# Performance work log

Hardware: AMD Instinct MI355X
Metric: run time of the kernel (lower is better)

## Reference

```python
import jax, jax.numpy as jnp
import numpy as np

D_MODEL = 1024
NUM_HEADS = 16
D_K = D_MODEL // NUM_HEADS


def setup_inputs() -> dict:
    key = jax.random.key(0)
    k1, k2, k3, kq, kk, kv, ko = jax.random.split(key, 7)
    B, S = 4, 2048
    scale = 1.0 / np.sqrt(D_MODEL)
    return {
        "Q_in": jax.random.normal(k1, (B, S, D_MODEL), dtype=jnp.float32),
        "K_in": jax.random.normal(k2, (B, S, D_MODEL), dtype=jnp.float32),
        "V_in": jax.random.normal(k3, (B, S, D_MODEL), dtype=jnp.float32),
        "W_q": jax.random.normal(kq, (D_MODEL, D_MODEL), dtype=jnp.float32) * scale,
        "W_k": jax.random.normal(kk, (D_MODEL, D_MODEL), dtype=jnp.float32) * scale,
        "W_v": jax.random.normal(kv, (D_MODEL, D_MODEL), dtype=jnp.float32) * scale,
        "W_o": jax.random.normal(ko, (D_MODEL, D_MODEL), dtype=jnp.float32) * scale,
    }


def _split_heads(x):
    B, S, _ = x.shape
    return x.reshape(B, S, NUM_HEADS, D_K).transpose(0, 2, 1, 3)  # [B,H,S,d_k]


def reference(Q_in, K_in, V_in, W_q, W_k, W_v, W_o):
    # nn.Linear: y = x @ W.T ; here W_* stored as [out, in] equivalent square,
    # use x @ W.T convention to match torch.
    Q = _split_heads(Q_in @ W_q.T)
    K = _split_heads(K_in @ W_k.T)
    V = _split_heads(V_in @ W_v.T)
    scores = jnp.einsum("bhqd,bhkd->bhqk", Q, K) / jnp.sqrt(jnp.float32(D_K))
    attn = jax.nn.softmax(scores, axis=-1)  # [B,H,S,S]
    out = jnp.einsum("bhqk,bhkd->bhqd", attn, V)
    B, H, S, dk = out.shape
    concat = out.transpose(0, 2, 1, 3).reshape(B, S, H * dk)
    return concat @ W_o.T
```

## Files before the change

kernel.cpp:

```cpp
#include <hip/hip_runtime.h>
#include <math.h>

typedef __bf16 bf16x8v __attribute__((ext_vector_type(8)));
typedef float f32x4 __attribute__((ext_vector_type(4)));
typedef float f32x16 __attribute__((ext_vector_type(16)));

__device__ __forceinline__ void async_copy16(void* lds, const void* g) {
  __builtin_amdgcn_global_load_lds(
      (const __attribute__((address_space(1))) void*)g,
      (__attribute__((address_space(3))) void*)lds, 16, 0, 0);
}

struct CastArgs {
  const float* s[7];
  __bf16* d[7];
};
__global__ __launch_bounds__(256) void cast_kernel(CastArgs a) {
  const int t = blockIdx.y;
  const int n = (t < 3) ? 8388608 : 1048576;
  const int i = (blockIdx.x * 256 + threadIdx.x) * 8;
  if (i >= n) return;
  const float4 v0 = *(const float4*)(a.s[t] + i);
  const float4 v1 = *(const float4*)(a.s[t] + i + 4);
  bf16x8v o;
  o[0] = (__bf16)v0.x; o[1] = (__bf16)v0.y; o[2] = (__bf16)v0.z; o[3] = (__bf16)v0.w;
  o[4] = (__bf16)v1.x; o[5] = (__bf16)v1.y; o[6] = (__bf16)v1.z; o[7] = (__bf16)v1.w;
  *(bf16x8v*)(a.d[t] + i) = o;
}

template <int MODE, typename OutT>
__global__ __launch_bounds__(256) void gemm_bt(const __bf16* A, const __bf16* B,
                                               OutT* C,
                                               const __bf16* A2, const __bf16* B2,
                                               OutT* C2,
                                               int M, int N, int K) {
  __shared__ __bf16 As[128 * 64];
  __shared__ __bf16 Bs[128 * 64];
  if (blockIdx.z == 1) { A = A2; B = B2; C = C2; }
  const int tid = threadIdx.x;
  const int wave = tid >> 6, lane = tid & 63;
  const int lgrp = lane >> 4, lmod = lane & 15;
  const int bm = (MODE == 3 ? blockIdx.y : blockIdx.x) * 128;
  const int bn = (MODE == 3 ? blockIdx.x : blockIdx.y) * 128;
  const int wm = (wave >> 1) * 64, wn = (wave & 1) * 64;

  f32x4 acc[4][4];
#pragma unroll
  for (int mi = 0; mi < 4; mi++)
#pragma unroll
    for (int ni = 0; ni < 4; ni++)
#pragma unroll
      for (int r = 0; r < 4; r++) acc[mi][ni][r] = 0.f;

  for (int kt = 0; kt < K; kt += 64) {
#pragma unroll
    for (int i = 0; i < 4; i++) {
      const int s = i * 256 + tid;
      const int r = s >> 3, cb = s & 7;
      const int gc = (cb ^ (r & 7)) * 8;
      async_copy16(&As[s * 8], &A[(size_t)(bm + r) * K + kt + gc]);
      async_copy16(&Bs[s * 8], &B[(size_t)(bn + r) * K + kt + gc]);
    }
    __syncthreads();
#pragma unroll
    for (int ks = 0; ks < 2; ks++) {
      bf16x8v af[4], bf[4];
#pragma unroll
      for (int mi = 0; mi < 4; mi++) {
        const int row = wm + mi * 16 + lmod;
        af[mi] = *(const bf16x8v*)&As[row * 64 + ((ks * 4 + lgrp) ^ (row & 7)) * 8];
      }
#pragma unroll
      for (int ni = 0; ni < 4; ni++) {
        const int row = wn + ni * 16 + lmod;
        bf[ni] = *(const bf16x8v*)&Bs[row * 64 + ((ks * 4 + lgrp) ^ (row & 7)) * 8];
      }
#pragma unroll
      for (int mi = 0; mi < 4; mi++)
#pragma unroll
        for (int ni = 0; ni < 4; ni++)
          acc[mi][ni] = __builtin_amdgcn_mfma_f32_16x16x32_bf16(af[mi], bf[ni],
                                                                acc[mi][ni], 0, 0, 0);
    }
    __syncthreads();
  }

#pragma unroll
  for (int mi = 0; mi < 4; mi++)
#pragma unroll
    for (int ni = 0; ni < 4; ni++)
#pragma unroll
      for (int r = 0; r < 4; r++) {
        const int row = bm + wm + mi * 16 + lgrp * 4 + r;
        const int col = bn + wn + ni * 16 + lmod;
        if (MODE == 0) {
          C[(size_t)row * N + col] = (OutT)acc[mi][ni][r];
        } else if (MODE == 1) {
          C[(size_t)(row >> 11) * 2097152 + (size_t)(col >> 6) * 131072 +
            (size_t)(row & 2047) * 64 + (col & 63)] = (OutT)acc[mi][ni][r];
        } else {
          C[(size_t)(col >> 11) * 2097152 + (size_t)(row >> 6) * 131072 +
            (size_t)(row & 63) * 2048 + (col & 2047)] = (OutT)acc[mi][ni][r];
        }
      }
}

__global__ __launch_bounds__(256) void attn_kernel(const __bf16* __restrict__ Qh,
                                                   const __bf16* __restrict__ Kh,
                                                   const __bf16* __restrict__ Vt,
                                                   __bf16* __restrict__ O) {
  __shared__ __bf16 Ks0[64 * 64];
  __shared__ __bf16 Ks1[64 * 64];
  __shared__ __bf16 Vts0[64 * 64];
  __shared__ __bf16 Vts1[64 * 64];

  const int tid = threadIdx.x;
  const int wave = tid >> 6, lane = tid & 63;
  const int l31 = lane & 31, hi = lane >> 5;
  const int qt = blockIdx.y, y = blockIdx.x;
  const size_t hb = (size_t)y * 131072;
  const __bf16* Qb = Qh + hb + (size_t)qt * 128 * 64;
  const __bf16* Kb = Kh + hb;
  const __bf16* Vb = Vt + hb;
  const int wq0 = wave * 32;

  const int s0 = tid, s1 = 256 + tid;
  const int kr0 = s0 >> 3, kc0 = s0 & 7;
  const int kr1 = s1 >> 3, kc1 = s1 & 7;
  const __bf16* kSrc0 = Kb + (size_t)kr0 * 64 + (kc0 ^ (kr0 & 7)) * 8;
  const __bf16* kSrc1 = Kb + (size_t)kr1 * 64 + (kc1 ^ (kr1 & 7)) * 8;
  const __bf16* vSrc0 = Vb + (size_t)kr0 * 2048 + (kc0 ^ (kr0 & 7)) * 8;
  const __bf16* vSrc1 = Vb + (size_t)kr1 * 2048 + (kc1 ^ (kr1 & 7)) * 8;

  const float qscale = 0.125f * 1.44269504f;
  bf16x8v qf[4];
#pragma unroll
  for (int ks = 0; ks < 4; ks++) {
    bf16x8v q = *(const bf16x8v*)&Qb[(wq0 + l31) * 64 + ks * 16 + hi * 8];
#pragma unroll
    for (int j = 0; j < 8; j++) q[j] = (__bf16)((float)q[j] * qscale);
    qf[ks] = q;
  }

  float m_run = -INFINITY;
  float l_run = 0.f;
  f32x16 oacc[2];
#pragma unroll
  for (int nd = 0; nd < 2; nd++)
#pragma unroll
    for (int r = 0; r < 16; r++) oacc[nd][r] = 0.f;

  auto STAGE = [&](int c, __bf16* Kd, __bf16* Vd) {
    async_copy16(&Kd[s0 * 8], kSrc0 + (size_t)c * 4096);
    async_copy16(&Kd[s1 * 8], kSrc1 + (size_t)c * 4096);
    async_copy16(&Vd[s0 * 8], vSrc0 + (size_t)c * 64);
    async_copy16(&Vd[s1 * 8], vSrc1 + (size_t)c * 64);
  };

  auto COMPUTE = [&](const __bf16* Kbuf, const __bf16* Vbuf) {
    f32x16 st[2];
#pragma unroll
    for (int kvt = 0; kvt < 2; kvt++)
#pragma unroll
      for (int r = 0; r < 16; r++) st[kvt][r] = 0.f;
#pragma unroll
    for (int ks = 0; ks < 4; ks++) {
      const int sl = ((ks * 2 + hi) ^ (l31 & 7)) * 8;
      const bf16x8v kf0 = *(const bf16x8v*)&Kbuf[l31 * 64 + sl];
      const bf16x8v kf1 = *(const bf16x8v*)&Kbuf[(32 + l31) * 64 + sl];
      __builtin_amdgcn_s_setprio(1);
      st[0] = __builtin_amdgcn_mfma_f32_32x32x16_bf16(kf0, qf[ks], st[0], 0, 0, 0);
      st[1] = __builtin_amdgcn_mfma_f32_32x32x16_bf16(kf1, qf[ks], st[1], 0, 0, 0);
      __builtin_amdgcn_s_setprio(0);
    }

    float bmax[16];
#pragma unroll
    for (int j = 0; j < 16; j++) bmax[j] = fmaxf(st[0][j], st[1][j]);
#pragma unroll
    for (int s = 8; s > 0; s >>= 1)
#pragma unroll
      for (int j = 0; j < 8; j++)
        if (j < s) bmax[j] = fmaxf(bmax[j], bmax[j + s]);
    float rmax = bmax[0];
    rmax = fmaxf(rmax, __shfl_xor(rmax, 32));

    if (!__all(rmax - m_run <= 8.f)) {
      const float mnew = fmaxf(m_run, rmax);
      const float alpha = __builtin_amdgcn_exp2f(m_run - mnew);
      m_run = mnew;
      l_run *= alpha;
#pragma unroll
      for (int r = 0; r < 16; r++) {
        const float ar = __shfl(alpha, (r & 3) + 8 * (r >> 2) + 4 * hi);
        oacc[0][r] *= ar;
        oacc[1][r] *= ar;
      }
    }

    float psum = 0.f;
#pragma unroll
    for (int kvt = 0; kvt < 2; kvt++) {
#pragma unroll
      for (int sub = 0; sub < 2; sub++) {
        const int ks2 = kvt * 2 + sub;
        const int vs = ((ks2 * 2 + hi) ^ (l31 & 7)) * 8;
        const bf16x8v vf0 = *(const bf16x8v*)&Vbuf[l31 * 64 + vs];
        const bf16x8v vf1 = *(const bf16x8v*)&Vbuf[(32 + l31) * 64 + vs];
        const int o = sub * 8;
        float p[8];
#pragma unroll
        for (int j = 0; j < 8; j++) {
          p[j] = __builtin_amdgcn_exp2f(st[kvt][o + j] - m_run);
          psum += p[j];
        }
        unsigned x0, y0, x1, y1;
        asm("v_cvt_pk_bf16_f32 %0, %1, %2" : "=v"(x0) : "v"(p[0]), "v"(p[1]));
        asm("v_cvt_pk_bf16_f32 %0, %1, %2" : "=v"(y0) : "v"(p[4]), "v"(p[5]));
        asm("v_cvt_pk_bf16_f32 %0, %1, %2" : "=v"(x1) : "v"(p[2]), "v"(p[3]));
        asm("v_cvt_pk_bf16_f32 %0, %1, %2" : "=v"(y1) : "v"(p[6]), "v"(p[7]));
        asm("v_permlane32_swap_b32 %0, %1" : "+v"(x0), "+v"(y0));
        asm("v_permlane32_swap_b32 %0, %1" : "+v"(x1), "+v"(y1));
        union { unsigned u[4]; bf16x8v v; } af;
        af.u[0] = x0; af.u[1] = x1; af.u[2] = y0; af.u[3] = y1;
        __builtin_amdgcn_s_setprio(1);
        oacc[0] = __builtin_amdgcn_mfma_f32_32x32x16_bf16(af.v, vf0, oacc[0], 0, 0, 0);
        oacc[1] = __builtin_amdgcn_mfma_f32_32x32x16_bf16(af.v, vf1, oacc[1], 0, 0, 0);
        __builtin_amdgcn_s_setprio(0);
      }
    }
    l_run += psum;
  };

  STAGE(0, Ks0, Vts0);
  __syncthreads();
#pragma unroll 1
  for (int t = 0; t < 15; t++) {
    STAGE(2 * t + 1, Ks1, Vts1);
    COMPUTE(Ks0, Vts0);
    __syncthreads();
    STAGE(2 * t + 2, Ks0, Vts0);
    COMPUTE(Ks1, Vts1);
    __syncthreads();
  }
  STAGE(31, Ks1, Vts1);
  COMPUTE(Ks0, Vts0);
  __syncthreads();
  COMPUTE(Ks1, Vts1);

  l_run += __shfl_xor(l_run, 32);
  const float linv = 1.f / l_run;
  const int b = y >> 4, h = y & 15;
#pragma unroll
  for (int r = 0; r < 16; r++) {
    const int q = (r & 3) + 8 * (r >> 2) + 4 * hi;
    const float inv = __shfl(linv, q);
    const int srow = qt * 128 + wq0 + q;
    const size_t base = ((size_t)(b * 2048 + srow)) * 1024 + h * 64;
    O[base + l31] = (__bf16)(oacc[0][r] * inv);
    O[base + 32 + l31] = (__bf16)(oacc[1][r] * inv);
  }
}

extern "C" void kernel_launch(void* const* d_in, const int* in_sizes, int n_in,
                              void* d_out, int out_size, void* d_ws, size_t ws_size,
                              hipStream_t stream) {
  const float* Qin = (const float*)d_in[0];
  const float* Kin = (const float*)d_in[1];
  const float* Vin = (const float*)d_in[2];
  const float* Wq = (const float*)d_in[3];
  const float* Wk = (const float*)d_in[4];
  const float* Wv = (const float*)d_in[5];
  const float* Wo = (const float*)d_in[6];
  float* out = (float*)d_out;

  __bf16* base = (__bf16*)d_ws;
  __bf16* Qbf = base;
  __bf16* Kbf = base + 8388608;
  __bf16* Vbf = base + 16777216;
  __bf16* Wqb = base + 25165824;
  __bf16* Wkb = base + 26214400;
  __bf16* Wvb = base + 27262976;
  __bf16* Wob = base + 28311552;
  __bf16* Qh = base + 29360128;
  __bf16* Kh = base + 37748736;
  __bf16* Vt = base + 46137344;
  __bf16* AO = Qbf;

  CastArgs ca;
  ca.s[0] = Qin; ca.s[1] = Kin; ca.s[2] = Vin;
  ca.s[3] = Wq;  ca.s[4] = Wk;  ca.s[5] = Wv;  ca.s[6] = Wo;
  ca.d[0] = Qbf; ca.d[1] = Kbf; ca.d[2] = Vbf;
  ca.d[3] = Wqb; ca.d[4] = Wkb; ca.d[5] = Wvb; ca.d[6] = Wob;
  cast_kernel<<<dim3(4096, 7), 256, 0, stream>>>(ca);

  const int M = 8192, N = 1024, K = 1024;
  dim3 bb(256);
  gemm_bt<1, __bf16><<<dim3(64, 8, 2), bb, 0, stream>>>(Qbf, Wqb, Qh,
                                                        Kbf, Wkb, Kh, M, N, K);
  gemm_bt<3, __bf16><<<dim3(64, 8), bb, 0, stream>>>(Wvb, Vbf, Vt,
                                                     nullptr, nullptr, nullptr,
                                                     1024, 8192, K);
  attn_kernel<<<dim3(64, 16), bb, 0, stream>>>(Qh, Kh, Vt, AO);
  gemm_bt<0, float><<<dim3(64, 8), bb, 0, stream>>>(AO, Wob, out,
                                                    nullptr, nullptr, nullptr,
                                                    M, N, K);
}
```

Before: 338.6 us.

## Double-buffer LDS tiles in projection GEMM to overlap loads with MFMA

The GEMM kernel now uses two LDS buffers and issues the async global-to-LDS copies for the next K tile before computing on the current one. This hides global load latency behind matrix math, which the single-buffered loop exposed at every iteration. The K loop is hard-coded to 16 tiles of 64, so it assumes K=1024, and LDS use doubles, which may lower occupancy.

Result: faster. 329.7 us (-2.6%).

```diff
diff --git a/kernel.cpp b/kernel.cpp
--- a/kernel.cpp
+++ b/kernel.cpp
@@ -34,8 +34,10 @@
                                                const __bf16* A2, const __bf16* B2,
                                                OutT* C2,
                                                int M, int N, int K) {
-  __shared__ __bf16 As[128 * 64];
-  __shared__ __bf16 Bs[128 * 64];
+  __shared__ __bf16 As0[128 * 64];
+  __shared__ __bf16 Bs0[128 * 64];
+  __shared__ __bf16 As1[128 * 64];
+  __shared__ __bf16 Bs1[128 * 64];
   if (blockIdx.z == 1) { A = A2; B = B2; C = C2; }
   const int tid = threadIdx.x;
   const int wave = tid >> 6, lane = tid & 63;
@@ -44,6 +46,19 @@
   const int bn = (MODE == 3 ? blockIdx.x : blockIdx.y) * 128;
   const int wm = (wave >> 1) * 64, wn = (wave & 1) * 64;
 
+  const __bf16* aSrc[4];
+  const __bf16* bSrc[4];
+  int slot[4];
+#pragma unroll
+  for (int i = 0; i < 4; i++) {
+    const int s = i * 256 + tid;
+    const int r = s >> 3, cb = s & 7;
+    const int gc = (cb ^ (r & 7)) * 8;
+    slot[i] = s * 8;
+    aSrc[i] = A + (size_t)(bm + r) * K + gc;
+    bSrc[i] = B + (size_t)(bn + r) * K + gc;
+  }
+
   f32x4 acc[4][4];
 #pragma unroll
   for (int mi = 0; mi < 4; mi++)
@@ -52,28 +67,27 @@
 #pragma unroll
       for (int r = 0; r < 4; r++) acc[mi][ni][r] = 0.f;
 
-  for (int kt = 0; kt < K; kt += 64) {
+  auto STAGE = [&](int c, __bf16* Ad, __bf16* Bd) {
 #pragma unroll
     for (int i = 0; i < 4; i++) {
-      const int s = i * 256 + tid;
-      const int r = s >> 3, cb = s & 7;
-      const int gc = (cb ^ (r & 7)) * 8;
-      async_copy16(&As[s * 8], &A[(size_t)(bm + r) * K + kt + gc]);
-      async_copy16(&Bs[s * 8], &B[(size_t)(bn + r) * K + kt + gc]);
-    }
-    __syncthreads();
+      async_copy16(&Ad[slot[i]], aSrc[i] + (size_t)c * 64);
+      async_copy16(&Bd[slot[i]], bSrc[i] + (size_t)c * 64);
+    }
+  };
+
+  auto COMPUTE = [&](const __bf16* Abuf, const __bf16* Bbuf) {
 #pragma unroll
     for (int ks = 0; ks < 2; ks++) {
       bf16x8v af[4], bf[4];
 #pragma unroll
       for (int mi = 0; mi < 4; mi++) {
         const int row = wm + mi * 16 + lmod;
-        af[mi] = *(const bf16x8v*)&As[row * 64 + ((ks * 4 + lgrp) ^ (row & 7)) * 8];
+        af[mi] = *(const bf16x8v*)&Abuf[row * 64 + ((ks * 4 + lgrp) ^ (row & 7)) * 8];
       }
 #pragma unroll
       for (int ni = 0; ni < 4; ni++) {
         const int row = wn + ni * 16 + lmod;
-        bf[ni] = *(const bf16x8v*)&Bs[row * 64 + ((ks * 4 + lgrp) ^ (row & 7)) * 8];
+        bf[ni] = *(const bf16x8v*)&Bbuf[row * 64 + ((ks * 4 + lgrp) ^ (row & 7)) * 8];
       }
 #pragma unroll
       for (int mi = 0; mi < 4; mi++)
@@ -82,8 +96,23 @@
           acc[mi][ni] = __builtin_amdgcn_mfma_f32_16x16x32_bf16(af[mi], bf[ni],
                                                                 acc[mi][ni], 0, 0, 0);
     }
+  };
+
+  STAGE(0, As0, Bs0);
+  __syncthreads();
+#pragma unroll 1
+  for (int t = 0; t < 7; t++) {
+    STAGE(2 * t + 1, As1, Bs1);
+    COMPUTE(As0, Bs0);
     __syncthreads();
-  }
+    STAGE(2 * t + 2, As0, Bs0);
+    COMPUTE(As1, Bs1);
+    __syncthreads();
+  }
+  STAGE(15, As1, Bs1);
+  COMPUTE(As0, Bs0);
+  __syncthreads();
+  COMPUTE(As1, Bs1);
 
 #pragma unroll
   for (int mi = 0; mi < 4; mi++)
```
